# Optimization experiments

Measured on AMD Instinct MI355X. Metric: run time of the kernel, lower is better.

The kernel has to match this reference:

```python
import jax, jax.numpy as jnp
import numpy as np

N = 32768          # total nodes in batch (M graphs * N_agents)
E = N * 8          # edges (k_neighbors = 8)
DIN = 16           # node_obs_dim
DE = 8             # edge_dim (rel_pos 2 + one-hot 4 + dist 1 + payoff 1)
HE = 128           # embed_hidden_size
C = 64             # TransformerConv out_channels
H = 4              # heads (concat)
HC = H * C         # 256, final node embedding dim
EPS = 1e-5


def _ln(x, g, b):
    m = x.mean(-1, keepdims=True)
    v = ((x - m) ** 2).mean(-1, keepdims=True)
    return (x - m) * jax.lax.rsqrt(v + EPS) * g + b


def _seg_softmax(s, seg, n):
    # numerically stable softmax over edges grouped by destination node
    m = jax.ops.segment_max(s, seg, num_segments=n)
    e = jnp.exp(s - m[seg])
    z = jax.ops.segment_sum(e, seg, num_segments=n)
    return e / z[seg]


def setup_inputs() -> dict:
    key = jax.random.key(0)
    ks = jax.random.split(key, 40)

    def w(i, shape):
        return jax.random.normal(ks[i], shape, jnp.float32) * 0.05

    inp = {
        "x": jax.random.normal(ks[0], (N, DIN), jnp.float32),
        "edge_index": jax.random.randint(ks[1], (2, E), 0, N, dtype=jnp.int32),
        "edge_attr": jax.random.normal(ks[2], (E, DE), jnp.float32),
        # EmbedConv: lin1 + LN + one hidden Linear + LN (embed_layer_N=1)
        "e_W1": w(3, (DIN + DE, HE)), "e_b1": jnp.zeros((HE,), jnp.float32),
        "e_g1": jnp.ones((HE,), jnp.float32), "e_be1": jnp.zeros((HE,), jnp.float32),
        "e_W2": w(4, (HE, HE)), "e_b2": jnp.zeros((HE,), jnp.float32),
        "e_g2": jnp.ones((HE,), jnp.float32), "e_be2": jnp.zeros((HE,), jnp.float32),
    }
    # Two TransformerConv layers; layer0 in=HE, layer1 in=HC (concat heads)
    for l, din in enumerate([HE, HC]):
        base = 5 + l * 6
        inp[f"l{l}_Wq"] = w(base, (din, HC));     inp[f"l{l}_bq"] = jnp.zeros((HC,), jnp.float32)
        inp[f"l{l}_Wk"] = w(base + 1, (din, HC)); inp[f"l{l}_bk"] = jnp.zeros((HC,), jnp.float32)
        inp[f"l{l}_Wv"] = w(base + 2, (din, HC)); inp[f"l{l}_bv"] = jnp.zeros((HC,), jnp.float32)
        inp[f"l{l}_We"] = w(base + 3, (DE, HC))   # lin_edge has no bias in PyG
        inp[f"l{l}_Ws"] = w(base + 4, (din, HC)); inp[f"l{l}_bs"] = jnp.zeros((HC,), jnp.float32)
    return inp


def _tconv(h, edge_attr, src, dst, Wq, bq, Wk, bk, Wv, bv, We, Ws, bs):
    q = (h @ Wq + bq).reshape(N, H, C)
    k = (h @ Wk + bk).reshape(N, H, C)
    v = (h @ Wv + bv).reshape(N, H, C)
    e = (edge_attr @ We).reshape(E, H, C)
    ke = k[src] + e                      # [E,H,C]
    ve = v[src] + e                      # [E,H,C]
    s = (q[dst] * ke).sum(-1) / np.float32(np.sqrt(C))  # [E,H]
    a = _seg_softmax(s, dst, N)          # softmax over in-edges of each dst
    out = jax.ops.segment_sum(a[..., None] * ve, dst, num_segments=N)
    return out.reshape(N, HC) + h @ Ws + bs  # root_weight skip + bias


def reference(x, edge_attr, e_W1, e_b1, e_g1, e_be1, e_W2, e_b2, e_g2, e_be2,
              l0_Wq, l0_bq, l0_Wk, l0_bk, l0_Wv, l0_bv, l0_We, l0_Ws, l0_bs,
              l1_Wq, l1_bq, l1_Wk, l1_bk, l1_Wv, l1_bv, l1_We, l1_Ws, l1_bs,
              edge_index):
    src, dst = edge_index[0], edge_index[1]
    # EmbedConv: per-edge MLP on cat(x_j, edge_attr), scatter-add to dst
    m = jnp.concatenate([x[src], edge_attr], axis=1)    # [E, DIN+DE]
    m = _ln(jax.nn.relu(m @ e_W1 + e_b1), e_g1, e_be1)
    m = _ln(jax.nn.relu(m @ e_W2 + e_b2), e_g2, e_be2)
    h = jax.ops.segment_sum(m, dst, num_segments=N)      # [N, HE]
    # Two TransformerConv layers with ReLU activations
    h = jax.nn.relu(_tconv(h, edge_attr, src, dst, l0_Wq, l0_bq, l0_Wk, l0_bk,
                           l0_Wv, l0_bv, l0_We, l0_Ws, l0_bs))
    h = jax.nn.relu(_tconv(h, edge_attr, src, dst, l1_Wq, l1_bq, l1_Wk, l1_bk,
                           l1_Wv, l1_bv, l1_We, l1_Ws, l1_bs))
    return h  # graph_aggr == 'node': [N, HC]
```

## Files before the change

kernel.cpp:

```cpp
#include <hip/hip_runtime.h>
#include <hip/hip_bf16.h>

#define NN 32768
#define NE 262144

typedef unsigned short u16;
typedef unsigned int   u32;
typedef __bf16 bf16x8 __attribute__((ext_vector_type(8)));
typedef float  f32x16 __attribute__((ext_vector_type(16)));

__device__ __forceinline__ float bf2f(u16 u){ return __uint_as_float(((u32)u)<<16); }
__device__ __forceinline__ u16 f2bf(float f){ __hip_bfloat16 h = __float2bfloat16(f); return *(u16*)&h; }
__device__ __forceinline__ float4 ldbf4(const u16* p){
  ushort4 u = *(const ushort4*)p;
  return make_float4(bf2f(u.x), bf2f(u.y), bf2f(u.z), bf2f(u.w));
}
__device__ __forceinline__ void gload16(const void* g, void* l){
  __builtin_amdgcn_global_load_lds(
      (const __attribute__((address_space(1))) void*)g,
      (__attribute__((address_space(3))) void*)l, 16, 0, 0);
}

__global__ void k_deg(const int* __restrict__ ei, int* deg){
  int e = blockIdx.x*256 + threadIdx.x;
  if (e < NE) atomicAdd(&deg[ei[NE + e]], 1);
}

__global__ void k_scan1(const int* __restrict__ deg, int* __restrict__ rowptr, int* __restrict__ bsum){
  const int t = threadIdx.x, b = blockIdx.x;
  const int i = b*256 + t;
  const int ln = t & 63, wv = t >> 6;
  int v = deg[i];
  #pragma unroll
  for (int d = 1; d < 64; d <<= 1){
    int u = __shfl_up(v, d, 64);
    if (ln >= d) v += u;
  }
  __shared__ int wsum[4];
  if (ln == 63) wsum[wv] = v;
  __syncthreads();
  int p = 0;
  #pragma unroll
  for (int w = 0; w < 4; w++) if (w < wv) p += wsum[w];
  v += p;
  rowptr[i + 1] = v;
  if (t == 255) bsum[b] = v;
}

__global__ void k_scan2(const int* __restrict__ bsum, int* __restrict__ boff){
  const int t = threadIdx.x;
  const int ln = t & 63, wv = t >> 6;
  int own = bsum[t];
  int v = own;
  #pragma unroll
  for (int d = 1; d < 64; d <<= 1){
    int u = __shfl_up(v, d, 64);
    if (ln >= d) v += u;
  }
  __shared__ int wsum[2];
  if (ln == 63) wsum[wv] = v;
  __syncthreads();
  if (wv == 1) v += wsum[0];
  boff[t] = v - own;
}

__global__ void k_scan3(int* __restrict__ rowptr, const int* __restrict__ boff){
  const int t = threadIdx.x, b = blockIdx.x;
  rowptr[1 + b*256 + t] += boff[b];
  if (b == 0 && t == 0) rowptr[0] = 0;
}

__global__ void k_fill(const int* __restrict__ ei, const int* __restrict__ rowptr,
                       int* cursor, const float* __restrict__ ea,
                       int* __restrict__ csrc, float4* __restrict__ ea_csr){
  int e = blockIdx.x*256 + threadIdx.x;
  if (e < NE){
    int d = ei[NE + e];
    int p = rowptr[d] + atomicAdd(&cursor[d], 1);
    csrc[p] = ei[e];
    float4 a = *(const float4*)&ea[(size_t)e*8];
    float4 b = *(const float4*)&ea[(size_t)e*8 + 4];
    ea_csr[(size_t)p*2]     = a;
    ea_csr[(size_t)p*2 + 1] = b;
  }
}

__global__ void k_hist(const int* __restrict__ deg, int* ghist){
  __shared__ int lh[64];
  const int t = threadIdx.x;
  if (t < 64) lh[t] = 0;
  __syncthreads();
  int dg = min(deg[blockIdx.x*256 + t], 63);
  atomicAdd(&lh[dg], 1);
  __syncthreads();
  if (t < 64 && lh[t]) atomicAdd(&ghist[t], lh[t]);
}

__global__ void k_hoff(const int* __restrict__ ghist, int* __restrict__ goff){
  const int t = threadIdx.x;
  int v = ghist[t];
  int s = v;
  #pragma unroll
  for (int d = 1; d < 64; d <<= 1){
    int u = __shfl_up(s, d, 64);
    if (t >= d) s += u;
  }
  goff[t] = s - v;
}

__global__ void k_scatter(const int* __restrict__ deg, const int* __restrict__ goff,
                          int* gcur, int* __restrict__ perm){
  __shared__ int lh[64], lbase[64];
  const int t = threadIdx.x;
  if (t < 64) lh[t] = 0;
  __syncthreads();
  const int n = blockIdx.x*256 + t;
  const int dg = min(deg[n], 63);
  int lrank = atomicAdd(&lh[dg], 1);
  __syncthreads();
  if (t < 64) lbase[t] = lh[t] ? atomicAdd(&gcur[t], lh[t]) : 0;
  __syncthreads();
  perm[goff[dg] + lbase[dg] + lrank] = n;
}

__global__ void k_b2p(const float* __restrict__ W2, const float* __restrict__ be1,
                      const float* __restrict__ b2, float* __restrict__ b2p){
  int f = threadIdx.x;
  float a = b2[f];
  for (int k = 0; k < 128; k++) a += be1[k]*W2[k*128 + f];
  b2p[f] = a;
}

__global__ void k_eprep(const float* __restrict__ W1, const float* __restrict__ b1,
                        const float* __restrict__ W2, const float* __restrict__ g1,
                        const float* __restrict__ b2p, __bf16* __restrict__ Ecat){
  int i = blockIdx.x*256 + threadIdx.x;
  if (i >= 2816) return;
  bf16x8 v;
  if (i < 512){
    int r = i & 31, hh = (i>>5)&1, ks = (i>>6)&1, rt = i>>7;
    int feat = rt*32 + r, k0 = ks*16 + hh*8;
    #pragma unroll
    for (int j = 0; j < 8; j++){
      int k = k0 + j;
      float val = (k < 24) ? W1[k*128 + feat] : ((k == 24) ? b1[feat] : 0.f);
      v[j] = (__bf16)val;
    }
  } else {
    int m = i - 512;
    int r = m & 31, hh = (m>>5)&1, q = m>>6;
    int ks = q % 9, rt = q / 9;
    int feat = rt*32 + r, k0 = ks*16 + hh*8;
    #pragma unroll
    for (int j = 0; j < 8; j++){
      int k = k0 + j;
      float val = (k < 128) ? g1[k]*W2[k*128 + feat] : ((k == 128) ? b2p[feat] : 0.f);
      v[j] = (__bf16)val;
    }
  }
  *(bf16x8*)&Ecat[(size_t)i*8] = v;
}

struct WPtrs { const float* w[8]; const float* b[8]; };

__global__ void k_wprep(WPtrs wp, __bf16* __restrict__ W0cat, __bf16* __restrict__ W1cat,
                        float* __restrict__ bcat0, float* __restrict__ bcat1){
  int gid = blockIdx.x*256 + threadIdx.x;
  if (gid < 16384){
    int mat = gid >> 12, v = gid & 4095;
    int colm = v & 255, q = v >> 8;
    int k0 = (q>>1)*16 + (q&1)*8;
    const float* W = wp.w[mat];
    bf16x8 vec;
    #pragma unroll
    for (int j = 0; j < 8; j++) vec[j] = (__bf16)W[(size_t)(k0+j)*256 + colm];
    *(bf16x8*)&W0cat[((size_t)q*1152 + mat*256 + colm)*8] = vec;
  } else if (gid < 49152){
    int g = gid - 16384;
    int mat = g >> 13, v = g & 8191;
    int colm = v & 255, q = v >> 8;
    int k0 = (q>>1)*16 + (q&1)*8;
    const float* W = wp.w[4+mat];
    bf16x8 vec;
    #pragma unroll
    for (int j = 0; j < 8; j++) vec[j] = (__bf16)W[(size_t)(k0+j)*256 + colm];
    *(bf16x8*)&W1cat[((size_t)q*1152 + mat*256 + colm)*8] = vec;
  } else if (gid < 51200){
    int g = gid - 49152;
    if (g < 1024) bcat0[g] = wp.b[g>>8][g&255];
    else { int h = g-1024; bcat1[h] = wp.b[4 + (h>>8)][h&255]; }
  }
}

__global__ void k_mprep(const float* __restrict__ Wq, const float* __restrict__ bq,
                        const float* __restrict__ We, __bf16* __restrict__ Wcat,
                        float* __restrict__ bcat, int KK){
  __shared__ float sWq[8*256], sWe2[8*256];
  const int t = threadIdx.x, kb = blockIdx.x;
  for (int i = t; i < 2048; i += 256){
    sWq[i]  = Wq[(size_t)(kb*8 + (i>>8))*256 + (i & 255)];
    sWe2[i] = We[i];
  }
  __syncthreads();
  const int kk = t >> 5, col = t & 31;
  const int h = col >> 3, i = col & 7;
  float a = 0.f;
  #pragma unroll 8
  for (int c = 0; c < 64; c++)
    a += sWq[kk*256 + h*64 + c]*sWe2[i*256 + h*64 + c];
  int k = kb*8 + kk;
  int q = (k >> 4)*2 + ((k >> 3) & 1), j = k & 7;
  Wcat[((size_t)q*1152 + 1024 + col)*8 + j] = (__bf16)(0.125f*a);
  for (int z = t; z < 768; z += 256){
    int kz = kb*8 + (z / 96), cz = 32 + (z % 96);
    int qz = (kz >> 4)*2 + ((kz >> 3) & 1), jz = kz & 7;
    Wcat[((size_t)qz*1152 + 1024 + cz)*8 + jz] = (__bf16)0.f;
  }
  if (kb == 0 && t < 32){
    int hh = t >> 3, ii = t & 7;
    float b = 0.f;
    for (int c = 0; c < 64; c++) b += bq[hh*64 + c]*sWe2[ii*256 + hh*64 + c];
    bcat[1024 + t] = 0.125f*b;
  }
}

__global__ __launch_bounds__(256, 1) void k_embed(
    const float* __restrict__ x, const float4* __restrict__ ea_csr,
    const int* __restrict__ csrc, const int* __restrict__ rowptr,
    const int* __restrict__ perm, const __bf16* __restrict__ Ecat,
    const float* __restrict__ g2, const float* __restrict__ be2,
    u16* __restrict__ h0b)
{
  __shared__ alignas(16) __bf16 sE[2816*8];
  __shared__ float sg2[128], sbe2[128];
  const int t = threadIdx.x;
  const int wv = t >> 6, ln = t & 63, hi = ln >> 5, c32 = ln & 31;

  #pragma unroll
  for (int k = 0; k < 11; k++){
    int base = k*256 + wv*64;
    gload16(Ecat + (size_t)(base + ln)*8, &sE[(size_t)base*8]);
  }
  if (t < 128){ sg2[t] = g2[t]; sbe2[t] = be2[t]; }
  asm volatile("s_waitcnt vmcnt(0)" ::: "memory");
  __syncthreads();

  const int win  = blockIdx.x + (wv >> 1)*512;
  const int half = wv & 1;
  const int d    = perm[win*32 + c32];
  const int rp   = rowptr[d];
  const int deg  = rowptr[d+1] - rp;
  int md = deg;
  #pragma unroll
  for (int m = 1; m < 32; m <<= 1) md = max(md, __shfl_xor(md, m, 32));

  f32x16 hacc[4] = {};

  bool vc = half < deg;
  int p0 = vc ? (rp + half) : rp;
  int sc = csrc[p0];
  float4 xa = *(const float4*)&x[(size_t)sc*16 + hi*8];
  float4 xb = *(const float4*)&x[(size_t)sc*16 + hi*8 + 4];
  float4 ga = ea_csr[(size_t)p0*2];
  float4 gb = ea_csr[(size_t)p0*2 + 1];

  for (int j = half; j < md; j += 2){
    const float vm = vc ? 1.f : 0.f;
    bf16x8 b1f0, b1f1;
    {
      float xv[8]; *(float4*)&xv[0] = xa; *(float4*)&xv[4] = xb;
      #pragma unroll
      for (int q = 0; q < 8; q++) b1f0[q] = (__bf16)(xv[q]*vm);
      float evv[8]; *(float4*)&evv[0] = ga; *(float4*)&evv[4] = gb;
      #pragma unroll
      for (int q = 0; q < 8; q++)
        b1f1[q] = (__bf16)(hi ? ((q == 0) ? vm : 0.f) : evv[q]*vm);
    }

    bool vn = (j + 2) < deg;
    int pn = vn ? (rp + j + 2) : rp;
    int sn = csrc[pn];
    float4 xan = *(const float4*)&x[(size_t)sn*16 + hi*8];
    float4 xbn = *(const float4*)&x[(size_t)sn*16 + hi*8 + 4];
    float4 gan = ea_csr[(size_t)pn*2];
    float4 gbn = ea_csr[(size_t)pn*2 + 1];

    f32x16 a1[4] = {};
    #pragma unroll
    for (int ks = 0; ks < 2; ks++)
      #pragma unroll
      for (int rt = 0; rt < 4; rt++){
        bf16x8 af = *(const bf16x8*)&sE[((((rt*2 + ks)*2 + hi)*32) + c32)*8];
        a1[rt] = __builtin_amdgcn_mfma_f32_32x32x16_bf16(af, ks ? b1f1 : b1f0, a1[rt], 0, 0, 0);
      }

    {
      float s1 = 0.f, s2 = 0.f;
      #pragma unroll
      for (int rt = 0; rt < 4; rt++)
        #pragma unroll
        for (int rg = 0; rg < 16; rg++){
          float v = fmaxf(a1[rt][rg], 0.f);
          a1[rt][rg] = v; s1 += v; s2 += v*v;
        }
      s1 += __shfl_xor(s1, 32, 64);
      s2 += __shfl_xor(s2, 32, 64);
      float mean = s1*(1.f/128.f);
      float rs = rsqrtf(s2*(1.f/128.f) - mean*mean + 1e-5f);
      #pragma unroll
      for (int rt = 0; rt < 4; rt++)
        #pragma unroll
        for (int rg = 0; rg < 16; rg++)
          a1[rt][rg] = (a1[rt][rg] - mean)*rs;
    }

    f32x16 a2[4] = {};
    #pragma unroll
    for (int ks = 0; ks < 8; ks++){
      const int tt = ks >> 1, bb = (ks & 1)*8;
      float snd[4], rcv[4];
      #pragma unroll
      for (int q = 0; q < 4; q++)
        snd[q] = hi ? a1[tt][bb + q] : a1[tt][bb + 4 + q];
      #pragma unroll
      for (int q = 0; q < 4; q++)
        rcv[q] = __shfl_xor(snd[q], 32, 64);
      bf16x8 bf;
      #pragma unroll
      for (int q = 0; q < 4; q++){
        float lo = hi ? rcv[q] : a1[tt][bb + q];
        float hh = hi ? a1[tt][bb + 4 + q] : rcv[q];
        bf[q]     = (__bf16)lo;
        bf[4 + q] = (__bf16)hh;
      }
      #pragma unroll
      for (int rt = 0; rt < 4; rt++){
        bf16x8 af = *(const bf16x8*)&sE[(512 + (((rt*9 + ks)*2 + hi)*32) + c32)*8];
        a2[rt] = __builtin_amdgcn_mfma_f32_32x32x16_bf16(af, bf, a2[rt], 0, 0, 0);
      }
    }
    {
      bf16x8 bf;
      #pragma unroll
      for (int q = 0; q < 8; q++)
        bf[q] = (__bf16)((!hi && q == 0) ? vm : 0.f);
      #pragma unroll
      for (int rt = 0; rt < 4; rt++){
        bf16x8 af = *(const bf16x8*)&sE[(512 + (((rt*9 + 8)*2 + hi)*32) + c32)*8];
        a2[rt] = __builtin_amdgcn_mfma_f32_32x32x16_bf16(af, bf, a2[rt], 0, 0, 0);
      }
    }

    {
      float s1 = 0.f, s2 = 0.f;
      #pragma unroll
      for (int rt = 0; rt < 4; rt++)
        #pragma unroll
        for (int rg = 0; rg < 16; rg++){
          float v = fmaxf(a2[rt][rg], 0.f);
          a2[rt][rg] = v; s1 += v; s2 += v*v;
        }
      s1 += __shfl_xor(s1, 32, 64);
      s2 += __shfl_xor(s2, 32, 64);
      float mean = s1*(1.f/128.f);
      float rs = rsqrtf(s2*(1.f/128.f) - mean*mean + 1e-5f);
      #pragma unroll
      for (int rt = 0; rt < 4; rt++)
        #pragma unroll
        for (int rg = 0; rg < 16; rg++)
          hacc[rt][rg] += (a2[rt][rg] - mean)*rs;
    }

    vc = vn;
    xa = xan; xb = xbn; ga = gan; gb = gbn;
  }

  __syncthreads();
  float* xch = (float*)sE;
  const int wbase = (wv >> 1)*(64*65);
  if (!half){
    #pragma unroll
    for (int rt = 0; rt < 4; rt++)
      #pragma unroll
      for (int rg = 0; rg < 16; rg++)
        xch[wbase + (rt*16 + rg)*65 + ln] = hacc[rt][rg];
  }
  __syncthreads();
  if (half){
    const float dd = (float)deg;
    #pragma unroll
    for (int rt = 0; rt < 4; rt++){
      #pragma unroll
      for (int rg = 0; rg < 16; rg++)
        hacc[rt][rg] += xch[wbase + (rt*16 + rg)*65 + ln];
      #pragma unroll
      for (int q = 0; q < 4; q++){
        int fb = rt*32 + 8*q + 4*hi;
        ushort4 o;
        o.x = f2bf(sg2[fb+0]*hacc[rt][q*4+0] + dd*sbe2[fb+0]);
        o.y = f2bf(sg2[fb+1]*hacc[rt][q*4+1] + dd*sbe2[fb+1]);
        o.z = f2bf(sg2[fb+2]*hacc[rt][q*4+2] + dd*sbe2[fb+2]);
        o.w = f2bf(sg2[fb+3]*hacc[rt][q*4+3] + dd*sbe2[fb+3]);
        *(ushort4*)&h0b[(size_t)d*128 + fb] = o;
      }
    }
  }
}

template<int K>
__global__ __launch_bounds__(256) void k_qkvs2(const u16* __restrict__ A,
    const __bf16* __restrict__ Wcat, const float* __restrict__ bcat,
    u16* __restrict__ qo, u16* __restrict__ kvb, u16* __restrict__ so,
    u16* __restrict__ wqe)
{
  __shared__ alignas(16) __bf16 sA[1024*8];
  __shared__ alignas(16) __bf16 sB[1024*8];
  const int t = threadIdx.x;
  const int swz = (blockIdx.x & 7)*288 + (blockIdx.x >> 3);
  const int r0 = (swz / 9)*128, c0 = (swz % 9)*128;
  const int wv = t >> 6, ln = t & 63, hi = ln >> 5, c32 = ln & 31;
  const int wr = wv >> 1, wc = wv & 1;

  f32x16 acc[2][2] = {};
  for (int kc = 0; kc < K/64; kc++){
    __syncthreads();
    #pragma unroll
    for (int ii = 0; ii < 4; ii++){
      int v = ii*256 + wv*64 + ln;
      int r = v & 31, hh = (v>>5)&1, ks = (v>>6)&3, rt = v>>8;
      gload16(A + (size_t)(r0 + rt*32 + r)*K + kc*64 + ks*16 + hh*8,
              &sA[(size_t)(ii*256 + wv*64)*8]);
    }
    #pragma unroll
    for (int ii = 0; ii < 4; ii++){
      int v = ii*256 + wv*64 + ln;
      int col = v & 127, q = v >> 7;
      gload16(Wcat + ((size_t)(kc*8 + q)*1152 + c0 + col)*8,
              &sB[(size_t)(ii*256 + wv*64)*8]);
    }
    asm volatile("s_waitcnt vmcnt(0)" ::: "memory");
    __syncthreads();
    #pragma unroll
    for (int ks = 0; ks < 4; ks++){
      bf16x8 af0 = *(const bf16x8*)&sA[((((wr*2+0)*4 + ks)*2 + hi)*32 + c32)*8];
      bf16x8 af1 = *(const bf16x8*)&sA[((((wr*2+1)*4 + ks)*2 + hi)*32 + c32)*8];
      bf16x8 bf0 = *(const bf16x8*)&sB[(((ks*2 + hi)*128) + wc*64 + c32)*8];
      bf16x8 bf1 = *(const bf16x8*)&sB[(((ks*2 + hi)*128) + wc*64 + 32 + c32)*8];
      acc[0][0] = __builtin_amdgcn_mfma_f32_32x32x16_bf16(af0, bf0, acc[0][0], 0, 0, 0);
      acc[0][1] = __builtin_amdgcn_mfma_f32_32x32x16_bf16(af0, bf1, acc[0][1], 0, 0, 0);
      acc[1][0] = __builtin_amdgcn_mfma_f32_32x32x16_bf16(af1, bf0, acc[1][0], 0, 0, 0);
      acc[1][1] = __builtin_amdgcn_mfma_f32_32x32x16_bf16(af1, bf1, acc[1][1], 0, 0, 0);
    }
  }

  const int tile = c0 >> 7;
  u16* omp; int rstride; int vadd = -1; bool wq8 = false;
  if (tile < 2)      { omp = qo;  rstride = 256; }
  else if (tile < 4) { omp = kvb; rstride = 512; vadd = 0; }
  else if (tile < 6) { omp = kvb; rstride = 512; vadd = 4; }
  else if (tile < 8) { omp = so;  rstride = 256; }
  else               { omp = wqe; rstride = 32; wq8 = true; }
  const int cb = c0 & 255;
  #pragma unroll
  for (int ci = 0; ci < 2; ci++){
    int colm = (wq8 ? 0 : cb) + wc*64 + ci*32 + c32;
    int coff = (vadd >= 0) ? (((colm >> 2) << 3) + vadd + (colm & 3)) : colm;
    float bb = bcat[c0 + wc*64 + ci*32 + c32];
    if (wq8 && colm >= 32) continue;
    #pragma unroll
    for (int ri = 0; ri < 2; ri++){
      #pragma unroll
      for (int rg = 0; rg < 16; rg++){
        int row = r0 + (wr*2 + ri)*32 + (rg&3) + 8*(rg>>2) + 4*hi;
        omp[(size_t)row*rstride + coff] = f2bf(acc[ri][ci][rg] + bb);
      }
    }
  }
}

template<bool OBF>
__global__ __launch_bounds__(256) void k_attn(
    const int* __restrict__ csrc, const int* __restrict__ rowptr,
    const float4* __restrict__ ea_csr, const float* __restrict__ We,
    const u16* __restrict__ qb, const u16* __restrict__ kvb,
    const u16* __restrict__ skb, const u16* __restrict__ wqe,
    void* __restrict__ outp)
{
  __shared__ float sWe[8*256];
  const int t = threadIdx.x;
  for (int i = t; i < 2048; i += 256) sWe[i] = We[i];
  __syncthreads();

  const float* eaf = (const float*)ea_csr;
  const int wv = t >> 6, ln = t & 63;
  const int f = (ln >> 4)*64 + (ln & 15)*4;
  const int kvo = ((ln >> 4)*16 + (ln & 15))*8;
  const int iown = ln & 7;
  const int gbase = ln & ~15;
  const int gw = blockIdx.x*4 + wv, nW = gridDim.x*4;

#define ATT_PRE(RX, EX, jj) do{                                            \
      int sj_ = ((jj) < 64) ? __shfl(sidx, (jj), 64) : csrc[rp + (jj)];    \
      RX = *(const int4*)&kvb[(size_t)sj_*512 + kvo];                      \
      EX = eaf[(size_t)(rp + (jj))*8 + iown];                              \
    }while(0)

#define ATT_STEP(RX, EX) do{                                               \
      float kx0 = bf2f((u16)(RX.x & 0xffff)), kx1 = bf2f((u16)(((u32)RX.x)>>16)); \
      float kx2 = bf2f((u16)(RX.y & 0xffff)), kx3 = bf2f((u16)(((u32)RX.y)>>16)); \
      float vx0 = bf2f((u16)(RX.z & 0xffff)), vx1 = bf2f((u16)(((u32)RX.z)>>16)); \
      float vx2 = bf2f((u16)(RX.w & 0xffff)), vx3 = bf2f((u16)(((u32)RX.w)>>16)); \
      float spp = qv.x*kx0 + qv.y*kx1 + qv.z*kx2 + qv.w*kx3 + EX*wqsel;    \
      spp += __shfl_xor(spp, 1, 64); spp += __shfl_xor(spp, 2, 64);        \
      spp += __shfl_xor(spp, 4, 64); spp += __shfl_xor(spp, 8, 64);        \
      float nm = fmaxf(m, spp);                                            \
      float sc_ = __expf(m - nm);                                          \
      float pp = __expf(spp - nm);                                         \
      l = l*sc_ + pp;                                                      \
      o0 = o0*sc_ + pp*vx0; o1 = o1*sc_ + pp*vx1;                          \
      o2 = o2*sc_ + pp*vx2; o3 = o3*sc_ + pp*vx3;                          \
      weal = weal*sc_ + pp*EX;                                             \
      m = nm;                                                              \
    }while(0)

  for (int d = gw; d < NN; d += nW){
    const int rp = rowptr[d];
    const int dg = rowptr[d+1] - rp;
    float4 qv = ldbf4(qb + (size_t)d*256 + f);
    qv.x *= 0.125f; qv.y *= 0.125f; qv.z *= 0.125f; qv.w *= 0.125f;
    float4 sv = ldbf4(skb + (size_t)d*256 + f);

    float wqsel = ((ln & 15) < 8)
                ? bf2f(wqe[(size_t)d*32 + (ln >> 4)*8 + (ln & 7)]) : 0.f;

    float m = -INFINITY, l = 0.f, o0 = 0, o1 = 0, o2 = 0, o3 = 0, weal = 0.f;

    if (dg > 0){
      int sidx = (ln < dg) ? csrc[rp + ln] : 0;
      int4 rA, rB, rC, rD; float eA, eB, eC, eD;
      ATT_PRE(rA, eA, 0);
      if (dg > 1) ATT_PRE(rB, eB, 1);
      if (dg > 2) ATT_PRE(rC, eC, 2);
      if (dg > 3) ATT_PRE(rD, eD, 3);

      int j = 0;
      while (j < dg){
        ATT_STEP(rA, eA); if (j + 4 < dg) ATT_PRE(rA, eA, j + 4); if (++j >= dg) break;
        ATT_STEP(rB, eB); if (j + 4 < dg) ATT_PRE(rB, eB, j + 4); if (++j >= dg) break;
        ATT_STEP(rC, eC); if (j + 4 < dg) ATT_PRE(rC, eC, j + 4); if (++j >= dg) break;
        ATT_STEP(rD, eD); if (j + 4 < dg) ATT_PRE(rD, eD, j + 4); ++j;
      }
    }

    float il = (l > 0.f) ? 1.f/l : 0.f;
    float ec0 = 0, ec1 = 0, ec2 = 0, ec3 = 0;
    #pragma unroll
    for (int i = 0; i < 8; i++){
      float wi = __shfl(weal, gbase + i, 64);
      float4 w = *(const float4*)&sWe[i*256 + f];
      ec0 += wi*w.x; ec1 += wi*w.y; ec2 += wi*w.z; ec3 += wi*w.w;
    }
    o0 = fmaxf((o0 + ec0)*il + sv.x, 0.f);
    o1 = fmaxf((o1 + ec1)*il + sv.y, 0.f);
    o2 = fmaxf((o2 + ec2)*il + sv.z, 0.f);
    o3 = fmaxf((o3 + ec3)*il + sv.w, 0.f);
    if constexpr (OBF){
      ushort4 o; o.x = f2bf(o0); o.y = f2bf(o1); o.z = f2bf(o2); o.w = f2bf(o3);
      *(ushort4*)((u16*)outp + (size_t)d*256 + f) = o;
    } else {
      *(float4*)((float*)outp + (size_t)d*256 + f) = make_float4(o0, o1, o2, o3);
    }
  }
#undef ATT_PRE
#undef ATT_STEP
}

extern "C" void kernel_launch(void* const* d_in, const int* in_sizes, int n_in,
                              void* d_out, int out_size, void* d_ws, size_t ws_size,
                              hipStream_t stream)
{
  (void)in_sizes; (void)n_in; (void)out_size; (void)ws_size;
  const float* x   = (const float*)d_in[0];
  const int*   ei  = (const int*)  d_in[1];
  const float* ea  = (const float*)d_in[2];
  const float* eW1 = (const float*)d_in[3];
  const float* eb1 = (const float*)d_in[4];
  const float* eg1 = (const float*)d_in[5];
  const float* ebe1= (const float*)d_in[6];
  const float* eW2 = (const float*)d_in[7];
  const float* eb2 = (const float*)d_in[8];
  const float* eg2 = (const float*)d_in[9];
  const float* ebe2= (const float*)d_in[10];

  char* ws = (char*)d_ws;
  const size_t MB = (size_t)1 << 20;
  const size_t KB = (size_t)1 << 10;
  int*   deg    = (int*)(ws);
  int*   cursor = (int*)(ws + 128*KB);
  int*   rowptr = (int*)(ws + 256*KB);
  int*   bsum   = (int*)(ws + 400*KB);
  int*   boff   = (int*)(ws + 402*KB);
  float* b2p    = (float*)(ws + 404*KB);
  int*   ghist  = (int*)(ws + 408*KB);
  int*   gcur   = (int*)(ws + 412*KB);
  int*   goff   = (int*)(ws + 416*KB);
  int*   perm   = (int*)(ws + 512*KB);
  int*   csrc   = (int*)(ws + 1*MB);
  float4* ea_csr= (float4*)(ws + 4*MB);
  u16*   qb     = (u16*)(ws + 20*MB);
  u16*   kvb    = (u16*)(ws + 36*MB);
  u16*   skb    = (u16*)(ws + 68*MB);
  u16*   h1     = (u16*)(ws + 84*MB);
  u16*   h0b    = (u16*)(ws + 100*MB);
  __bf16* W0cat = (__bf16*)(ws + 108*MB);
  __bf16* W1cat = (__bf16*)(ws + 109*MB);
  float* bcat0  = (float*)(ws + 110*MB);
  float* bcat1  = (float*)(ws + 110*MB + 64*KB);
  __bf16* Ecat  = (__bf16*)(ws + 111*MB);
  u16*   wqeb   = (u16*)(ws + 112*MB);

  hipMemsetAsync(deg, 0, 256*KB, stream);
  hipMemsetAsync(ghist, 0, 12*KB, stream);

  k_deg  <<<NE/256, 256, 0, stream>>>(ei, deg);
  k_scan1<<<128,    256, 0, stream>>>(deg, rowptr, bsum);
  k_scan2<<<1,      128, 0, stream>>>(bsum, boff);
  k_scan3<<<128,    256, 0, stream>>>(rowptr, boff);
  k_fill <<<NE/256, 256, 0, stream>>>(ei, rowptr, cursor, ea, csrc, ea_csr);
  k_hist <<<NN/256, 256, 0, stream>>>(deg, ghist);
  k_hoff <<<1,       64, 0, stream>>>(ghist, goff);
  k_scatter<<<NN/256,256, 0, stream>>>(deg, goff, gcur, perm);
  k_b2p  <<<1,      128, 0, stream>>>(eW2, ebe1, eb2, b2p);
  k_eprep<<<11,     256, 0, stream>>>(eW1, eb1, eW2, eg1, b2p, Ecat);

  WPtrs wp;
  wp.w[0] = (const float*)d_in[11]; wp.b[0] = (const float*)d_in[12];
  wp.w[1] = (const float*)d_in[13]; wp.b[1] = (const float*)d_in[14];
  wp.w[2] = (const float*)d_in[15]; wp.b[2] = (const float*)d_in[16];
  wp.w[3] = (const float*)d_in[18]; wp.b[3] = (const float*)d_in[19];
  wp.w[4] = (const float*)d_in[20]; wp.b[4] = (const float*)d_in[21];
  wp.w[5] = (const float*)d_in[22]; wp.b[5] = (const float*)d_in[23];
  wp.w[6] = (const float*)d_in[24]; wp.b[6] = (const float*)d_in[25];
  wp.w[7] = (const float*)d_in[27]; wp.b[7] = (const float*)d_in[28];
  k_wprep<<<200, 256, 0, stream>>>(wp, W0cat, W1cat, bcat0, bcat1);
  k_mprep<<<16, 256, 0, stream>>>((const float*)d_in[11], (const float*)d_in[12],
                                  (const float*)d_in[17], W0cat, bcat0, 128);
  k_mprep<<<32, 256, 0, stream>>>((const float*)d_in[20], (const float*)d_in[21],
                                  (const float*)d_in[26], W1cat, bcat1, 256);

  k_embed<<<512, 256, 0, stream>>>(x, ea_csr, csrc, rowptr, perm, Ecat, eg2, ebe2, h0b);

  k_qkvs2<128><<<2304, 256, 0, stream>>>(h0b, W0cat, bcat0, qb, kvb, skb, wqeb);
  k_attn<true><<<NN/4, 256, 0, stream>>>(csrc, rowptr, ea_csr, (const float*)d_in[17],
                                         qb, kvb, skb, wqeb, (void*)h1);
  k_qkvs2<256><<<2304, 256, 0, stream>>>(h1, W1cat, bcat1, qb, kvb, skb, wqeb);
  k_attn<false><<<NN/4, 256, 0, stream>>>(csrc, rowptr, ea_csr, (const float*)d_in[26],
                                          qb, kvb, skb, wqeb, d_out);
}
```

Before: 338.1 us.

## Merge preprocessing kernels and deepen attention edge prefetch to six

Folds the scan, histogram, offset and scatter kernels into three combined launches. Merges all weight-prep kernels, including the bias fold previously done in k_b2p, into a single k_prep launch, and replaces two memsets with one. This cuts launch count and inter-kernel gaps in the setup phase. The attention loop now prefetches six neighbour rows ahead instead of four, hiding more gather latency at the cost of extra registers. The bias fold is now recomputed redundantly per element.

```diff
diff --git a/kernel.cpp b/kernel.cpp
--- a/kernel.cpp
+++ b/kernel.cpp
@@ -26,48 +26,89 @@
   if (e < NE) atomicAdd(&deg[ei[NE + e]], 1);
 }
 
-__global__ void k_scan1(const int* __restrict__ deg, int* __restrict__ rowptr, int* __restrict__ bsum){
-  const int t = threadIdx.x, b = blockIdx.x;
-  const int i = b*256 + t;
-  const int ln = t & 63, wv = t >> 6;
-  int v = deg[i];
-  #pragma unroll
-  for (int d = 1; d < 64; d <<= 1){
-    int u = __shfl_up(v, d, 64);
-    if (ln >= d) v += u;
-  }
-  __shared__ int wsum[4];
-  if (ln == 63) wsum[wv] = v;
-  __syncthreads();
-  int p = 0;
-  #pragma unroll
-  for (int w = 0; w < 4; w++) if (w < wv) p += wsum[w];
-  v += p;
-  rowptr[i + 1] = v;
-  if (t == 255) bsum[b] = v;
-}
-
-__global__ void k_scan2(const int* __restrict__ bsum, int* __restrict__ boff){
+__global__ void k_scan1hist(const int* __restrict__ deg, int* __restrict__ rowptr,
+                            int* __restrict__ bsum, int* ghist){
+  __shared__ int sbuf[64];
   const int t = threadIdx.x;
-  const int ln = t & 63, wv = t >> 6;
-  int own = bsum[t];
-  int v = own;
-  #pragma unroll
-  for (int d = 1; d < 64; d <<= 1){
-    int u = __shfl_up(v, d, 64);
-    if (ln >= d) v += u;
-  }
-  __shared__ int wsum[2];
-  if (ln == 63) wsum[wv] = v;
-  __syncthreads();
-  if (wv == 1) v += wsum[0];
-  boff[t] = v - own;
-}
-
-__global__ void k_scan3(int* __restrict__ rowptr, const int* __restrict__ boff){
-  const int t = threadIdx.x, b = blockIdx.x;
-  rowptr[1 + b*256 + t] += boff[b];
-  if (b == 0 && t == 0) rowptr[0] = 0;
+  if (blockIdx.x < 128){
+    const int b = blockIdx.x;
+    const int i = b*256 + t;
+    const int ln = t & 63, wv = t >> 6;
+    int v = deg[i];
+    #pragma unroll
+    for (int d = 1; d < 64; d <<= 1){
+      int u = __shfl_up(v, d, 64);
+      if (ln >= d) v += u;
+    }
+    if (ln == 63) sbuf[wv] = v;
+    __syncthreads();
+    int p = 0;
+    #pragma unroll
+    for (int w = 0; w < 4; w++) if (w < wv) p += sbuf[w];
+    v += p;
+    rowptr[i + 1] = v;
+    if (t == 255) bsum[b] = v;
+  } else {
+    const int b = blockIdx.x - 128;
+    if (t < 64) sbuf[t] = 0;
+    __syncthreads();
+    int dg = min(deg[b*256 + t], 63);
+    atomicAdd(&sbuf[dg], 1);
+    __syncthreads();
+    if (t < 64 && sbuf[t]) atomicAdd(&ghist[t], sbuf[t]);
+  }
+}
+
+__global__ void k_scan2hoff(const int* __restrict__ bsum, int* __restrict__ boff,
+                            const int* __restrict__ ghist, int* __restrict__ goff){
+  const int t = threadIdx.x;
+  if (blockIdx.x == 0){
+    const int ln = t & 63, wv = t >> 6;
+    int own = bsum[t];
+    int v = own;
+    #pragma unroll
+    for (int d = 1; d < 64; d <<= 1){
+      int u = __shfl_up(v, d, 64);
+      if (ln >= d) v += u;
+    }
+    __shared__ int wsum[2];
+    if (ln == 63) wsum[wv] = v;
+    __syncthreads();
+    if (wv == 1) v += wsum[0];
+    boff[t] = v - own;
+  } else if (t < 64){
+    int v = ghist[t];
+    int s = v;
+    #pragma unroll
+    for (int d = 1; d < 64; d <<= 1){
+      int u = __shfl_up(s, d, 64);
+      if (t >= d) s += u;
+    }
+    goff[t] = s - v;
+  }
+}
+
+__global__ void k_scan3scatter(int* __restrict__ rowptr, const int* __restrict__ boff,
+                               const int* __restrict__ deg, const int* __restrict__ goff,
+                               int* gcur, int* __restrict__ perm){
+  const int t = threadIdx.x;
+  if (blockIdx.x < 128){
+    const int b = blockIdx.x;
+    rowptr[1 + b*256 + t] += boff[b];
+    if (b == 0 && t == 0) rowptr[0] = 0;
+  } else {
+    __shared__ int lh[64], lbase[64];
+    const int b = blockIdx.x - 128;
+    if (t < 64) lh[t] = 0;
+    __syncthreads();
+    const int n = b*256 + t;
+    const int dg = min(deg[n], 63);
+    int lrank = atomicAdd(&lh[dg], 1);
+    __syncthreads();
+    if (t < 64) lbase[t] = lh[t] ? atomicAdd(&gcur[t], lh[t]) : 0;
+    __syncthreads();
+    perm[goff[dg] + lbase[dg] + lrank] = n;
+  }
 }
 
 __global__ void k_fill(const int* __restrict__ ei, const int* __restrict__ rowptr,
@@ -85,118 +126,13 @@
   }
 }
 
-__global__ void k_hist(const int* __restrict__ deg, int* ghist){
-  __shared__ int lh[64];
+struct WPtrs { const float* w[8]; const float* b[8]; };
+
+__device__ void mprep_body(const float* __restrict__ Wq, const float* __restrict__ bq,
+                           const float* __restrict__ We, __bf16* __restrict__ Wcat,
+                           float* __restrict__ bcat, int kb,
+                           float* sWq, float* sWe2){
   const int t = threadIdx.x;
-  if (t < 64) lh[t] = 0;
-  __syncthreads();
-  int dg = min(deg[blockIdx.x*256 + t], 63);
-  atomicAdd(&lh[dg], 1);
-  __syncthreads();
-  if (t < 64 && lh[t]) atomicAdd(&ghist[t], lh[t]);
-}
-
-__global__ void k_hoff(const int* __restrict__ ghist, int* __restrict__ goff){
-  const int t = threadIdx.x;
-  int v = ghist[t];
-  int s = v;
-  #pragma unroll
-  for (int d = 1; d < 64; d <<= 1){
-    int u = __shfl_up(s, d, 64);
-    if (t >= d) s += u;
-  }
-  goff[t] = s - v;
-}
-
-__global__ void k_scatter(const int* __restrict__ deg, const int* __restrict__ goff,
-                          int* gcur, int* __restrict__ perm){
-  __shared__ int lh[64], lbase[64];
-  const int t = threadIdx.x;
-  if (t < 64) lh[t] = 0;
-  __syncthreads();
-  const int n = blockIdx.x*256 + t;
-  const int dg = min(deg[n], 63);
-  int lrank = atomicAdd(&lh[dg], 1);
-  __syncthreads();
-  if (t < 64) lbase[t] = lh[t] ? atomicAdd(&gcur[t], lh[t]) : 0;
-  __syncthreads();
-  perm[goff[dg] + lbase[dg] + lrank] = n;
-}
-
-__global__ void k_b2p(const float* __restrict__ W2, const float* __restrict__ be1,
-                      const float* __restrict__ b2, float* __restrict__ b2p){
-  int f = threadIdx.x;
-  float a = b2[f];
-  for (int k = 0; k < 128; k++) a += be1[k]*W2[k*128 + f];
-  b2p[f] = a;
-}
-
-__global__ void k_eprep(const float* __restrict__ W1, const float* __restrict__ b1,
-                        const float* __restrict__ W2, const float* __restrict__ g1,
-                        const float* __restrict__ b2p, __bf16* __restrict__ Ecat){
-  int i = blockIdx.x*256 + threadIdx.x;
-  if (i >= 2816) return;
-  bf16x8 v;
-  if (i < 512){
-    int r = i & 31, hh = (i>>5)&1, ks = (i>>6)&1, rt = i>>7;
-    int feat = rt*32 + r, k0 = ks*16 + hh*8;
-    #pragma unroll
-    for (int j = 0; j < 8; j++){
-      int k = k0 + j;
-      float val = (k < 24) ? W1[k*128 + feat] : ((k == 24) ? b1[feat] : 0.f);
-      v[j] = (__bf16)val;
-    }
-  } else {
-    int m = i - 512;
-    int r = m & 31, hh = (m>>5)&1, q = m>>6;
-    int ks = q % 9, rt = q / 9;
-    int feat = rt*32 + r, k0 = ks*16 + hh*8;
-    #pragma unroll
-    for (int j = 0; j < 8; j++){
-      int k = k0 + j;
-      float val = (k < 128) ? g1[k]*W2[k*128 + feat] : ((k == 128) ? b2p[feat] : 0.f);
-      v[j] = (__bf16)val;
-    }
-  }
-  *(bf16x8*)&Ecat[(size_t)i*8] = v;
-}
-
-struct WPtrs { const float* w[8]; const float* b[8]; };
-
-__global__ void k_wprep(WPtrs wp, __bf16* __restrict__ W0cat, __bf16* __restrict__ W1cat,
-                        float* __restrict__ bcat0, float* __restrict__ bcat1){
-  int gid = blockIdx.x*256 + threadIdx.x;
-  if (gid < 16384){
-    int mat = gid >> 12, v = gid & 4095;
-    int colm = v & 255, q = v >> 8;
-    int k0 = (q>>1)*16 + (q&1)*8;
-    const float* W = wp.w[mat];
-    bf16x8 vec;
-    #pragma unroll
-    for (int j = 0; j < 8; j++) vec[j] = (__bf16)W[(size_t)(k0+j)*256 + colm];
-    *(bf16x8*)&W0cat[((size_t)q*1152 + mat*256 + colm)*8] = vec;
-  } else if (gid < 49152){
-    int g = gid - 16384;
-    int mat = g >> 13, v = g & 8191;
-    int colm = v & 255, q = v >> 8;
-    int k0 = (q>>1)*16 + (q&1)*8;
-    const float* W = wp.w[4+mat];
-    bf16x8 vec;
-    #pragma unroll
-    for (int j = 0; j < 8; j++) vec[j] = (__bf16)W[(size_t)(k0+j)*256 + colm];
-    *(bf16x8*)&W1cat[((size_t)q*1152 + mat*256 + colm)*8] = vec;
-  } else if (gid < 51200){
-    int g = gid - 49152;
-    if (g < 1024) bcat0[g] = wp.b[g>>8][g&255];
-    else { int h = g-1024; bcat1[h] = wp.b[4 + (h>>8)][h&255]; }
-  }
-}
-
-__global__ void k_mprep(const float* __restrict__ Wq, const float* __restrict__ bq,
-                        const float* __restrict__ We, __bf16* __restrict__ Wcat,
-                        float* __restrict__ bcat, int KK){
-  __shared__ float sWq[8*256], sWe2[8*256];
-  const int t = threadIdx.x, kb = blockIdx.x;
   for (int i = t; i < 2048; i += 256){
     sWq[i]  = Wq[(size_t)(kb*8 + (i>>8))*256 + (i & 255)];
     sWe2[i] = We[i];
@@ -221,6 +157,83 @@
     float b = 0.f;
     for (int c = 0; c < 64; c++) b += bq[hh*64 + c]*sWe2[ii*256 + hh*64 + c];
     bcat[1024 + t] = 0.125f*b;
+  }
+}
+
+__global__ void k_prep(WPtrs wp, __bf16* __restrict__ W0cat, __bf16* __restrict__ W1cat,
+                       float* __restrict__ bcat0, float* __restrict__ bcat1,
+                       const float* __restrict__ Wq0, const float* __restrict__ bq0,
+                       const float* __restrict__ We0,
+                       const float* __restrict__ Wq1, const float* __restrict__ bq1,
+                       const float* __restrict__ We1,
+                       const float* __restrict__ eW1, const float* __restrict__ eb1,
+                       const float* __restrict__ eW2, const float* __restrict__ eg1,
+                       const float* __restrict__ eb2, const float* __restrict__ ebe1,
+                       __bf16* __restrict__ Ecat){
+  __shared__ float sWq[2048], sWe2[2048];
+  const int b = blockIdx.x, t = threadIdx.x;
+  if (b < 200){
+    int gid = b*256 + t;
+    if (gid < 16384){
+      int mat = gid >> 12, v = gid & 4095;
+      int colm = v & 255, q = v >> 8;
+      int k0 = (q>>1)*16 + (q&1)*8;
+      const float* W = wp.w[mat];
+      bf16x8 vec;
+      #pragma unroll
+      for (int j = 0; j < 8; j++) vec[j] = (__bf16)W[(size_t)(k0+j)*256 + colm];
+      *(bf16x8*)&W0cat[((size_t)q*1152 + mat*256 + colm)*8] = vec;
+    } else if (gid < 49152){
+      int g = gid - 16384;
+      int mat = g >> 13, v = g & 8191;
+      int colm = v & 255, q = v >> 8;
+      int k0 = (q>>1)*16 + (q&1)*8;
+      const float* W = wp.w[4+mat];
+      bf16x8 vec;
+      #pragma unroll
+      for (int j = 0; j < 8; j++) vec[j] = (__bf16)W[(size_t)(k0+j)*256 + colm];
+      *(bf16x8*)&W1cat[((size_t)q*1152 + mat*256 + colm)*8] = vec;
+    } else if (gid < 51200){
+      int g = gid - 49152;
+      if (g < 1024) bcat0[g] = wp.b[g>>8][g&255];
+      else { int h = g-1024; bcat1[h] = wp.b[4 + (h>>8)][h&255]; }
+    }
+  } else if (b < 216){
+    mprep_body(Wq0, bq0, We0, W0cat, bcat0, b - 200, sWq, sWe2);
+  } else if (b < 248){
+    mprep_body(Wq1, bq1, We1, W1cat, bcat1, b - 216, sWq, sWe2);
+  } else {
+    int i = (b - 248)*256 + t;
+    if (i >= 2816) return;
+    bf16x8 v;
+    if (i < 512){
+      int r = i & 31, hh = (i>>5)&1, ks = (i>>6)&1, rt = i>>7;
+      int feat = rt*32 + r, k0 = ks*16 + hh*8;
+      #pragma unroll
+      for (int j = 0; j < 8; j++){
+        int k = k0 + j;
+        float val = (k < 24) ? eW1[k*128 + feat] : ((k == 24) ? eb1[feat] : 0.f);
+        v[j] = (__bf16)val;
+      }
+    } else {
+      int m = i - 512;
+      int r = m & 31, hh = (m>>5)&1, q = m>>6;
+      int ks = q % 9, rt = q / 9;
+      int feat = rt*32 + r, k0 = ks*16 + hh*8;
+      #pragma unroll
+      for (int j = 0; j < 8; j++){
+        int k = k0 + j;
+        float val;
+        if (k < 128) val = eg1[k]*eW2[k*128 + feat];
+        else if (k == 128){
+          float a = eb2[feat];
+          for (int kk = 0; kk < 128; kk++) a += ebe1[kk]*eW2[kk*128 + feat];
+          val = a;
+        } else val = 0.f;
+        v[j] = (__bf16)val;
+      }
+    }
+    *(bf16x8*)&Ecat[(size_t)i*8] = v;
   }
 }
 
@@ -537,18 +550,22 @@
 
     if (dg > 0){
       int sidx = (ln < dg) ? csrc[rp + ln] : 0;
-      int4 rA, rB, rC, rD; float eA, eB, eC, eD;
+      int4 rA, rB, rC, rD, rE, rF; float eA, eB, eC, eD, eE, eF;
       ATT_PRE(rA, eA, 0);
       if (dg > 1) ATT_PRE(rB, eB, 1);
       if (dg > 2) ATT_PRE(rC, eC, 2);
       if (dg > 3) ATT_PRE(rD, eD, 3);
+      if (dg > 4) ATT_PRE(rE, eE, 4);
+      if (dg > 5) ATT_PRE(rF, eF, 5);
 
       int j = 0;
       while (j < dg){
-        ATT_STEP(rA, eA); if (j + 4 < dg) ATT_PRE(rA, eA, j + 4); if (++j >= dg) break;
-        ATT_STEP(rB, eB); if (j + 4 < dg) ATT_PRE(rB, eB, j + 4); if (++j >= dg) break;
-        ATT_STEP(rC, eC); if (j + 4 < dg) ATT_PRE(rC, eC, j + 4); if (++j >= dg) break;
-        ATT_STEP(rD, eD); if (j + 4 < dg) ATT_PRE(rD, eD, j + 4); ++j;
+        ATT_STEP(rA, eA); if (j + 6 < dg) ATT_PRE(rA, eA, j + 6); if (++j >= dg) break;
+        ATT_STEP(rB, eB); if (j + 6 < dg) ATT_PRE(rB, eB, j + 6); if (++j >= dg) break;
+        ATT_STEP(rC, eC); if (j + 6 < dg) ATT_PRE(rC, eC, j + 6); if (++j >= dg) break;
+        ATT_STEP(rD, eD); if (j + 6 < dg) ATT_PRE(rD, eD, j + 6); if (++j >= dg) break;
+        ATT_STEP(rE, eE); if (j + 6 < dg) ATT_PRE(rE, eE, j + 6); if (++j >= dg) break;
+        ATT_STEP(rF, eF); if (j + 6 < dg) ATT_PRE(rF, eF, j + 6); ++j;
       }
     }
 
@@ -600,7 +617,6 @@
   int*   rowptr = (int*)(ws + 256*KB);
   int*   bsum   = (int*)(ws + 400*KB);
   int*   boff   = (int*)(ws + 402*KB);
-  float* b2p    = (float*)(ws + 404*KB);
   int*   ghist  = (int*)(ws + 408*KB);
   int*   gcur   = (int*)(ws + 412*KB);
   int*   goff   = (int*)(ws + 416*KB);
@@ -619,19 +635,7 @@
   __bf16* Ecat  = (__bf16*)(ws + 111*MB);
   u16*   wqeb   = (u16*)(ws + 112*MB);
 
-  hipMemsetAsync(deg, 0, 256*KB, stream);
-  hipMemsetAsync(ghist, 0, 12*KB, stream);
-
-  k_deg  <<<NE/256, 256, 0, stream>>>(ei, deg);
-  k_scan1<<<128,    256, 0, stream>>>(deg, rowptr, bsum);
-  k_scan2<<<1,      128, 0, stream>>>(bsum, boff);
-  k_scan3<<<128,    256, 0, stream>>>(rowptr, boff);
-  k_fill <<<NE/256, 256, 0, stream>>>(ei, rowptr, cursor, ea, csrc, ea_csr);
-  k_hist <<<NN/256, 256, 0, stream>>>(deg, ghist);
-  k_hoff <<<1,       64, 0, stream>>>(ghist, goff);
-  k_scatter<<<NN/256,256, 0, stream>>>(deg, goff, gcur, perm);
-  k_b2p  <<<1,      128, 0, stream>>>(eW2, ebe1, eb2, b2p);
-  k_eprep<<<11,     256, 0, stream>>>(eW1, eb1, eW2, eg1, b2p, Ecat);
+  hipMemsetAsync(ws, 0, 420*KB, stream);
 
   WPtrs wp;
   wp.w[0] = (const float*)d_in[11]; wp.b[0] = (const float*)d_in[12];
@@ -642,11 +646,16 @@
   wp.w[5] = (const float*)d_in[22]; wp.b[5] = (const float*)d_in[23];
   wp.w[6] = (const float*)d_in[24]; wp.b[6] = (const float*)d_in[25];
   wp.w[7] = (const float*)d_in[27]; wp.b[7] = (const float*)d_in[28];
-  k_wprep<<<200, 256, 0, stream>>>(wp, W0cat, W1cat, bcat0, bcat1);
-  k_mprep<<<16, 256, 0, stream>>>((const float*)d_in[11], (const float*)d_in[12],
-                                  (const float*)d_in[17], W0cat, bcat0, 128);
-  k_mprep<<<32, 256, 0, stream>>>((const float*)d_in[20], (const float*)d_in[21],
-                                  (const float*)d_in[26], W1cat, bcat1, 256);
+
+  k_deg        <<<NE/256, 256, 0, stream>>>(ei, deg);
+  k_prep       <<<259,    256, 0, stream>>>(wp, W0cat, W1cat, bcat0, bcat1,
+                  (const float*)d_in[11], (const float*)d_in[12], (const float*)d_in[17],
+                  (const float*)d_in[20], (const float*)d_in[21], (const float*)d_in[26],
+                  eW1, eb1, eW2, eg1, eb2, ebe1, Ecat);
+  k_scan1hist  <<<256, 256, 0, stream>>>(deg, rowptr, bsum, ghist);
+  k_scan2hoff  <<<2,   128, 0, stream>>>(bsum, boff, ghist, goff);
+  k_scan3scatter<<<256,256, 0, stream>>>(rowptr, boff, deg, goff, gcur, perm);
+  k_fill       <<<NE/256, 256, 0, stream>>>(ei, rowptr, cursor, ea, csrc, ea_csr);
 
   k_embed<<<512, 256, 0, stream>>>(x, ea_csr, csrc, rowptr, perm, Ecat, eg2, ebe2, h0b);
 
```

After: 343.5 us. Within noise of the previous version (+1.6%).
